# Performance work log

Measured on AMD Instinct MI355X. Metric: run time of the kernel, lower is better.

The kernel has to match this reference:

```python
import jax, jax.numpy as jnp
import numpy as np

GAMMA = 0.99
NUM_CODEWORDS = 512
CODEBOOK_DIM = 64


def setup_inputs() -> dict:
    key = jax.random.key(0)
    kx, kc = jax.random.split(key)
    x = jax.random.normal(kx, (32, 64, 64, 64), dtype=jnp.float32)  # [N,C,H,W]
    codebook = jax.random.normal(kc, (NUM_CODEWORDS, CODEBOOK_DIM), dtype=jnp.float32) / 2
    N_state = jnp.ones((NUM_CODEWORDS,), dtype=jnp.float32)
    m_state = codebook.copy()
    return {"x": x, "codebook": codebook, "N_state": N_state, "m_state": m_state}


def reference(x, codebook, N_state, m_state):
    N, C, H, W = x.shape
    K = codebook.shape[0]
    # flatten to tokens: [N*H*W, C]
    xf = jnp.transpose(x, (0, 2, 3, 1)).reshape(-1, C)
    d2 = (jnp.sum(xf * xf, axis=-1, keepdims=True)
          - 2.0 * (xf @ codebook.T)
          + jnp.sum(codebook * codebook, axis=-1)[None, :])
    index = jnp.argmin(d2, axis=1)  # [T]
    q = codebook[index].reshape(N, H, W, C).transpose(0, 3, 1, 2)  # [N,C,H,W]
    # straight-through estimator
    out = x + jax.lax.stop_gradient(q - x)
    # EMA update (training path, no_grad in original)
    counts = jax.ops.segment_sum(jnp.ones_like(index, dtype=x.dtype), index, num_segments=K)
    sums = jax.ops.segment_sum(xf, index, num_segments=K)  # [K,C]
    occupied = counts > 0
    N_new = jnp.where(occupied, N_state * GAMMA + counts * (1.0 - GAMMA), N_state)
    m_new = jnp.where(occupied[:, None], m_state * GAMMA + sums * (1.0 - GAMMA), m_state)
    codebook_new = m_new / N_new[:, None]
    return out, codebook_new, N_new, m_new
```

## Files before the change

kernel.cpp:

```cpp
#include <hip/hip_runtime.h>

static constexpr int Nn_ = 32, Cc_ = 64, Hh_ = 64, Ww_ = 64;
static constexpr int K_ = 512;
static constexpr int HW_ = Hh_ * Ww_;
static constexpr int CHW_ = Cc_ * HW_;
static constexpr int T_ = Nn_ * Hh_ * Ww_;
static constexpr int OUT_ELEMS = Nn_ * Cc_ * Hh_ * Ww_;
static constexpr int OFF_CB = OUT_ELEMS;
static constexpr int OFF_N  = OUT_ELEMS + 32768;
static constexpr int OFF_M  = OUT_ELEMS + 32768 + 512;

static constexpr int WS_ACC  = 0;
static constexpr int ACC_CNT = 32768;
static constexpr int ACC_F   = K_ * Cc_ + K_;
static constexpr int ZERO4   = ACC_F / 4;

__global__ __launch_bounds__(256) void k_zero(float* __restrict__ ws) {
    int i = blockIdx.x * 256 + threadIdx.x;
    if (i < ZERO4) ((float4*)(ws + WS_ACC))[i] = make_float4(0.f, 0.f, 0.f, 0.f);
}

__global__ __launch_bounds__(256, 2) void k_assign(const float* __restrict__ x,
                                                   const float* __restrict__ cb,
                                                   float* __restrict__ ws,
                                                   float* __restrict__ out) {
    __shared__ alignas(16) float xs[64][132];
    __shared__ alignas(16) float cs[128][68];
    __shared__ float cnorm512[512];
    __shared__ int bi_s[128];

    const int b    = blockIdx.x;
    const int tid  = threadIdx.x;
    const int mg   = tid & 15;
    const int ng   = tid >> 4;
    const int lane = tid & 63;
    const int wv   = tid >> 6;
    const int row0 = 2 * b, row1 = 2 * b + 1;
    const int xb0 = (row0 >> 6) * CHW_ + (row0 & 63) * Ww_;
    const int xb1 = (row1 >> 6) * CHW_ + (row1 & 63) * Ww_;

#pragma unroll
    for (int stp = 0; stp < 8; ++stp) {
        int e = stp * 256 + tid;
        int c = e >> 5, s = e & 31;
        int r = s >> 4, wq = s & 15;
        float4 v = *(const float4*)(x + (r ? xb1 : xb0) + c * HW_ + 4 * wq);
        *(float4*)&xs[c][4 * s] = v;
    }

    for (int r = tid; r < 512; r += 256) {
        const float4* cr = (const float4*)(cb + r * 64);
        float a = 0.f;
#pragma unroll
        for (int i = 0; i < 16; ++i) {
            float4 v = cr[i];
            a = fmaf(v.x, v.x, a); a = fmaf(v.y, v.y, a);
            a = fmaf(v.z, v.z, a); a = fmaf(v.w, v.w, a);
        }
        cnorm512[r] = a;
    }

    float bdA[4], bdB[4];
    int   bkA[4], bkB[4];
#pragma unroll
    for (int i = 0; i < 4; ++i) {
        bdA[i] = __int_as_float(0x7f800000);
        bdB[i] = __int_as_float(0x7f800000);
        bkA[i] = 0; bkB[i] = 0;
    }

#pragma unroll 1
    for (int kt = 0; kt < 4; ++kt) {
#pragma unroll
        for (int stp = 0; stp < 8; ++stp) {
            int e = stp * 256 + tid;
            int rr = e >> 4, cq = e & 15;
            float4 v = *(const float4*)(cb + (kt * 128 + rr) * 64 + 4 * cq);
            *(float4*)&cs[rr][4 * cq] = v;
        }
        __syncthreads();

        float aAA[4][4], aAB[4][4], aBA[4][4], aBB[4][4];
#pragma unroll
        for (int a = 0; a < 4; ++a)
#pragma unroll
            for (int c2 = 0; c2 < 4; ++c2) {
                aAA[a][c2] = 0.f; aAB[a][c2] = 0.f;
                aBA[a][c2] = 0.f; aBB[a][c2] = 0.f;
            }

#pragma unroll 4
        for (int c4 = 0; c4 < 64; c4 += 4) {
            float xA[4][4], xB[4][4], cA[4][4], cB[4][4];
#pragma unroll
            for (int i = 0; i < 4; ++i) {
                *(float4*)xA[i] = *(const float4*)&xs[c4 + i][4 * mg];
                *(float4*)xB[i] = *(const float4*)&xs[c4 + i][64 + 4 * mg];
            }
#pragma unroll
            for (int j = 0; j < 4; ++j) {
                *(float4*)cA[j] = *(const float4*)&cs[4 * ng + j][c4];
                *(float4*)cB[j] = *(const float4*)&cs[64 + 4 * ng + j][c4];
            }
#pragma unroll
            for (int j = 0; j < 4; ++j)
#pragma unroll
                for (int mi = 0; mi < 4; ++mi)
#pragma unroll
                    for (int i = 0; i < 4; ++i) {
                        aAA[mi][j] = fmaf(xA[i][mi], cA[j][i], aAA[mi][j]);
                        aAB[mi][j] = fmaf(xA[i][mi], cB[j][i], aAB[mi][j]);
                        aBA[mi][j] = fmaf(xB[i][mi], cA[j][i], aBA[mi][j]);
                        aBB[mi][j] = fmaf(xB[i][mi], cB[j][i], aBB[mi][j]);
                    }
        }
        __syncthreads();

        const int kb = kt * 128 + 4 * ng;
#pragma unroll
        for (int j = 0; j < 4; ++j) {
            float cn = cnorm512[kb + j];
            int   kk = kb + j;
#pragma unroll
            for (int mi = 0; mi < 4; ++mi) {
                float dA = fmaf(-2.0f, aAA[mi][j], cn);
                if (dA < bdA[mi]) { bdA[mi] = dA; bkA[mi] = kk; }
                float dB = fmaf(-2.0f, aBA[mi][j], cn);
                if (dB < bdB[mi]) { bdB[mi] = dB; bkB[mi] = kk; }
            }
        }
#pragma unroll
        for (int j = 0; j < 4; ++j) {
            float cn = cnorm512[kb + 64 + j];
            int   kk = kb + 64 + j;
#pragma unroll
            for (int mi = 0; mi < 4; ++mi) {
                float dA = fmaf(-2.0f, aAB[mi][j], cn);
                if (dA < bdA[mi]) { bdA[mi] = dA; bkA[mi] = kk; }
                float dB = fmaf(-2.0f, aBB[mi][j], cn);
                if (dB < bdB[mi]) { bdB[mi] = dB; bkB[mi] = kk; }
            }
        }
    }

    unsigned long long* red = (unsigned long long*)&cs[0][0];
#pragma unroll
    for (int mi = 0; mi < 4; ++mi) {
        unsigned uA = __float_as_uint(bdA[mi]);
        uA = (uA & 0x80000000u) ? ~uA : (uA | 0x80000000u);
        red[(4 * mg + mi) * 17 + ng] = ((unsigned long long)uA << 32) | (unsigned)bkA[mi];
        unsigned uB = __float_as_uint(bdB[mi]);
        uB = (uB & 0x80000000u) ? ~uB : (uB | 0x80000000u);
        red[(64 + 4 * mg + mi) * 17 + ng] = ((unsigned long long)uB << 32) | (unsigned)bkB[mi];
    }
    __syncthreads();
    if (tid < 128) {
        unsigned long long bm = red[tid * 17 + 0];
#pragma unroll
        for (int j = 1; j < 16; ++j) {
            unsigned long long v = red[tid * 17 + j];
            if (v < bm) bm = v;
        }
        bi_s[tid] = (int)(bm & 0xffffffffu);
    }
    __syncthreads();

    float* acc = ws + WS_ACC;
#pragma unroll 4
    for (int jj = 0; jj < 32; ++jj) {
        int tt = wv * 32 + jj;
        atomicAdd(acc + bi_s[tt] * 64 + lane, xs[lane][tt]);
    }
    if (tid < 128) atomicAdd(acc + ACC_CNT + bi_s[tid], 1.0f);
    __syncthreads();

    float (*qt)[132] = xs;
#pragma unroll
    for (int jj = 0; jj < 32; ++jj) {
        int tt = wv * 32 + jj;
        qt[lane][tt] = cb[bi_s[tt] * 64 + lane];
    }
    __syncthreads();
#pragma unroll
    for (int r = 0; r < 2; ++r)
#pragma unroll
        for (int j = 0; j < 16; ++j) {
            int c = wv * 16 + j;
            out[(r ? xb1 : xb0) + c * HW_ + lane] = qt[c][64 * r + lane];
        }
}

__global__ __launch_bounds__(256) void k_final(const float* __restrict__ Ns,
                                               const float* __restrict__ ms,
                                               const float* __restrict__ ws,
                                               float* __restrict__ out) {
    int i = blockIdx.x * 256 + threadIdx.x;
    int k = i >> 6, c = i & 63;

    const float* acc = ws + WS_ACC;
    float s   = acc[i];
    float cnt = acc[ACC_CNT + k];

    const float gamma = 0.99f;
    const float omg   = (float)(1.0 - 0.99);

    bool occ = cnt > 0.0f;
    float Nv = Ns[k];
    float Nnew = occ ? (Nv * gamma + cnt * omg) : Nv;

    float mv = ms[i];
    float mnew = occ ? (mv * gamma + s * omg) : mv;

    out[OFF_CB + i] = mnew / Nnew;
    out[OFF_M  + i] = mnew;
    if (c == 0) out[OFF_N + k] = Nnew;
}

extern "C" void kernel_launch(void* const* d_in, const int* in_sizes, int n_in,
                              void* d_out, int out_size, void* d_ws, size_t ws_size,
                              hipStream_t stream) {
    const float* x  = (const float*)d_in[0];
    const float* cb = (const float*)d_in[1];
    const float* Ns = (const float*)d_in[2];
    const float* ms = (const float*)d_in[3];
    float* out = (float*)d_out;
    float* ws  = (float*)d_ws;

    hipLaunchKernelGGL(k_zero,   dim3(33),   dim3(256), 0, stream, ws);
    hipLaunchKernelGGL(k_assign, dim3(1024), dim3(256), 0, stream, x, cb, ws, out);
    hipLaunchKernelGGL(k_final,  dim3(128),  dim3(256), 0, stream, Ns, ms, ws, out);
}
```

Baseline: 217.3 us.

## Compute codeword distances with split-fp16 MFMA and exact fp32 fallback for ambiguous tokens

Replaces the fp32 FMA distance GEMM with 32x32x16 fp16 MFMA using hi/lo split operands (three products) to approximate fp32 dot products. Tokens whose best-vs-second margin is below a threshold are queued and re-evaluated exactly in fp32 by a new fix-up kernel. A prep kernel precomputes split codebook and norms. This aims to cut the compute-bound distance cost at the risk of extra launches and misassignment if the margin is too small.

New measurement: 256.0 us. 17.8% more time.

```diff
diff --git a/kernel.cpp b/kernel.cpp
--- a/kernel.cpp
+++ b/kernel.cpp
@@ -10,171 +10,190 @@
 static constexpr int OFF_N  = OUT_ELEMS + 32768;
 static constexpr int OFF_M  = OUT_ELEMS + 32768 + 512;
 
-static constexpr int WS_ACC  = 0;
-static constexpr int ACC_CNT = 32768;
-static constexpr int ACC_F   = K_ * Cc_ + K_;
-static constexpr int ZERO4   = ACC_F / 4;
+static constexpr int WS_ACC     = 0;
+static constexpr int ACC_CNT    = 32768;
+static constexpr int ACC_F      = K_ * Cc_ + K_;
+static constexpr int WS_FIXCNT  = 33280;
+static constexpr int WS_FIXLIST = 33284;
+static constexpr int WS_CBH     = WS_FIXLIST + T_;
+static constexpr int WS_CBL     = WS_CBH + 16384;
+static constexpr int WS_CN      = WS_CBL + 16384;
+static constexpr int WS_CNA     = WS_CN + 512;
+
+static constexpr float THETA = 0.015f;
+
+typedef _Float16 half8  __attribute__((ext_vector_type(8)));
+typedef float    f32x16 __attribute__((ext_vector_type(16)));
 
 __global__ __launch_bounds__(256) void k_zero(float* __restrict__ ws) {
     int i = blockIdx.x * 256 + threadIdx.x;
-    if (i < ZERO4) ((float4*)(ws + WS_ACC))[i] = make_float4(0.f, 0.f, 0.f, 0.f);
-}
-
-__global__ __launch_bounds__(256, 2) void k_assign(const float* __restrict__ x,
+    if (i < 8321) ((float4*)ws)[i] = make_float4(0.f, 0.f, 0.f, 0.f);
+}
+
+__global__ __launch_bounds__(256) void k_prep(const float* __restrict__ cb,
+                                              float* __restrict__ ws) {
+    int j = blockIdx.x * 256 + threadIdx.x;
+    float v = cb[j];
+    _Float16 h = (_Float16)v;
+    _Float16 lo = (_Float16)(v - (float)h);
+    ((_Float16*)(ws + WS_CBH))[j] = h;
+    ((_Float16*)(ws + WS_CBL))[j] = lo;
+    float sq = v * v;
+#pragma unroll
+    for (int m = 1; m < 64; m <<= 1) sq += __shfl_xor(sq, m);
+    if ((threadIdx.x & 63) == 0) {
+        int k = j >> 6;
+        ws[WS_CN + k] = sq;
+        int t = k >> 5, r5 = k & 31;
+        int hi = (r5 >> 2) & 1;
+        int reg = (r5 & 3) + 4 * (r5 >> 3);
+        ws[WS_CNA + hi * 256 + t * 16 + reg] = sq;
+    }
+}
+
+__global__ __launch_bounds__(256, 4) void k_assign(const float* __restrict__ x,
                                                    const float* __restrict__ cb,
                                                    float* __restrict__ ws,
                                                    float* __restrict__ out) {
-    __shared__ alignas(16) float xs[64][132];
-    __shared__ alignas(16) float cs[128][68];
-    __shared__ float cnorm512[512];
-    __shared__ int bi_s[128];
+    __shared__ alignas(16) unsigned char smem[35840];
+    int* bi_s   = (int*)(smem + 34816);
+    int* cert_s = (int*)(smem + 35328);
 
     const int b    = blockIdx.x;
     const int tid  = threadIdx.x;
-    const int mg   = tid & 15;
-    const int ng   = tid >> 4;
     const int lane = tid & 63;
     const int wv   = tid >> 6;
     const int row0 = 2 * b, row1 = 2 * b + 1;
     const int xb0 = (row0 >> 6) * CHW_ + (row0 & 63) * Ww_;
     const int xb1 = (row1 >> 6) * CHW_ + (row1 & 63) * Ww_;
 
-#pragma unroll
-    for (int stp = 0; stp < 8; ++stp) {
-        int e = stp * 256 + tid;
-        int c = e >> 5, s = e & 31;
-        int r = s >> 4, wq = s & 15;
-        float4 v = *(const float4*)(x + (r ? xb1 : xb0) + c * HW_ + 4 * wq);
-        *(float4*)&xs[c][4 * s] = v;
-    }
-
-    for (int r = tid; r < 512; r += 256) {
-        const float4* cr = (const float4*)(cb + r * 64);
-        float a = 0.f;
-#pragma unroll
-        for (int i = 0; i < 16; ++i) {
-            float4 v = cr[i];
-            a = fmaf(v.x, v.x, a); a = fmaf(v.y, v.y, a);
-            a = fmaf(v.z, v.z, a); a = fmaf(v.w, v.w, a);
-        }
-        cnorm512[r] = a;
-    }
-
-    float bdA[4], bdB[4];
-    int   bkA[4], bkB[4];
-#pragma unroll
-    for (int i = 0; i < 4; ++i) {
-        bdA[i] = __int_as_float(0x7f800000);
-        bdB[i] = __int_as_float(0x7f800000);
-        bkA[i] = 0; bkB[i] = 0;
-    }
+    {
+        const int s  = tid & 31;
+        const int c8 = tid >> 5;
+        const int r  = s >> 4, wq = s & 15;
+        half8 hp[4], lp[4];
+#pragma unroll
+        for (int stp = 0; stp < 8; ++stp) {
+            int ch = c8 * 8 + stp;
+            float4 v = *(const float4*)(x + (r ? xb1 : xb0) + ch * HW_ + 4 * wq);
+            float vv[4] = {v.x, v.y, v.z, v.w};
+#pragma unroll
+            for (int j = 0; j < 4; ++j) {
+                _Float16 h = (_Float16)vv[j];
+                _Float16 lo = (_Float16)(vv[j] - (float)h);
+                hp[j][stp] = h; lp[j][stp] = lo;
+            }
+        }
+        const int blk = c8 ^ (wq & 7);
+#pragma unroll
+        for (int j = 0; j < 4; ++j) {
+            int tt = 64 * r + 4 * wq + j;
+            *(half8*)(smem + tt * 128 + blk * 16) = hp[j];
+            *(half8*)(smem + 16384 + tt * 128 + blk * 16) = lp[j];
+        }
+        ((float*)(smem + 32768))[tid]       = ws[WS_CNA + tid];
+        ((float*)(smem + 32768))[tid + 256] = ws[WS_CNA + tid + 256];
+    }
+    __syncthreads();
+
+    const int tb = 32 * wv + (lane & 31);
+    const int hi = lane >> 5;
+    half8 bh[4], bl[4];
+    {
+        const int tsw = (tb >> 2) & 7;
+#pragma unroll
+        for (int ks = 0; ks < 4; ++ks) {
+            int blk = (2 * ks + hi) ^ tsw;
+            bh[ks] = *(const half8*)(smem + tb * 128 + blk * 16);
+            bl[ks] = *(const half8*)(smem + 16384 + tb * 128 + blk * 16);
+        }
+    }
+
+    const _Float16* __restrict__ cbh = (const _Float16*)(ws + WS_CBH);
+    const _Float16* __restrict__ cbl = (const _Float16*)(ws + WS_CBL);
+    const float* cnA = (const float*)(smem + 32768);
+    float bd1 = __int_as_float(0x7f800000);
+    float bd2 = __int_as_float(0x7f800000);
+    int bk1 = 0;
 
 #pragma unroll 1
-    for (int kt = 0; kt < 4; ++kt) {
-#pragma unroll
-        for (int stp = 0; stp < 8; ++stp) {
-            int e = stp * 256 + tid;
-            int rr = e >> 4, cq = e & 15;
-            float4 v = *(const float4*)(cb + (kt * 128 + rr) * 64 + 4 * cq);
-            *(float4*)&cs[rr][4 * cq] = v;
-        }
-        __syncthreads();
-
-        float aAA[4][4], aAB[4][4], aBA[4][4], aBB[4][4];
-#pragma unroll
-        for (int a = 0; a < 4; ++a)
-#pragma unroll
-            for (int c2 = 0; c2 < 4; ++c2) {
-                aAA[a][c2] = 0.f; aAB[a][c2] = 0.f;
-                aBA[a][c2] = 0.f; aBB[a][c2] = 0.f;
+    for (int t = 0; t < 16; ++t) {
+        const _Float16* ab = cbh + (t * 32 + (lane & 31)) * 64 + 8 * hi;
+        const _Float16* lb = cbl + (t * 32 + (lane & 31)) * 64 + 8 * hi;
+        half8 ah[4], al[4];
+#pragma unroll
+        for (int ks = 0; ks < 4; ++ks) {
+            ah[ks] = *(const half8*)(ab + ks * 16);
+            al[ks] = *(const half8*)(lb + ks * 16);
+        }
+        f32x16 acc = {0.f,0.f,0.f,0.f, 0.f,0.f,0.f,0.f,
+                      0.f,0.f,0.f,0.f, 0.f,0.f,0.f,0.f};
+#pragma unroll
+        for (int ks = 0; ks < 4; ++ks) {
+            acc = __builtin_amdgcn_mfma_f32_32x32x16_f16(ah[ks], bh[ks], acc, 0, 0, 0);
+            acc = __builtin_amdgcn_mfma_f32_32x32x16_f16(ah[ks], bl[ks], acc, 0, 0, 0);
+            acc = __builtin_amdgcn_mfma_f32_32x32x16_f16(al[ks], bh[ks], acc, 0, 0, 0);
+        }
+        float cnv[16];
+        {
+            const float* cnp = cnA + hi * 256 + t * 16;
+            *(float4*)&cnv[0]  = *(const float4*)(cnp);
+            *(float4*)&cnv[4]  = *(const float4*)(cnp + 4);
+            *(float4*)&cnv[8]  = *(const float4*)(cnp + 8);
+            *(float4*)&cnv[12] = *(const float4*)(cnp + 12);
+        }
+        const int tb16 = t << 4;
+#pragma unroll
+        for (int j = 0; j < 16; ++j) {
+            float d = fmaf(-2.0f, acc[j], cnv[j]);
+            int kid = tb16 | j;
+            bool lt = d < bd1;
+            bd2 = lt ? bd1 : fminf(bd2, d);
+            bk1 = lt ? kid : bk1;
+            bd1 = fminf(bd1, d);
+        }
+    }
+
+    {
+        int t0 = bk1 >> 4, j0 = bk1 & 15;
+        int rk = 32 * t0 + (j0 & 3) + 8 * (j0 >> 2) + 4 * hi;
+        unsigned uf = __float_as_uint(bd1);
+        uf = (uf & 0x80000000u) ? ~uf : (uf | 0x80000000u);
+        unsigned long long me = ((unsigned long long)uf << 32) | (unsigned)rk;
+        unsigned long long ot = (unsigned long long)__shfl_xor((long long)me, 32);
+        float od1 = __shfl_xor(bd1, 32);
+        float od2 = __shfl_xor(bd2, 32);
+        unsigned long long m1 = (me < ot) ? me : ot;
+        float d1m = fminf(bd1, od1);
+        float d2m = fminf(fminf(bd2, od2), fmaxf(bd1, od1));
+        if (hi == 0) {
+            int k1 = (int)(m1 & 0xffffffffu);
+            bool cert = (d2m - d1m) > THETA;
+            bi_s[tb] = k1;
+            cert_s[tb] = cert ? 1 : 0;
+            if (!cert) {
+                int pos = atomicAdd((int*)(ws + WS_FIXCNT), 1);
+                ((int*)(ws + WS_FIXLIST))[pos] = 128 * b + tb;
             }
-
-#pragma unroll 4
-        for (int c4 = 0; c4 < 64; c4 += 4) {
-            float xA[4][4], xB[4][4], cA[4][4], cB[4][4];
-#pragma unroll
-            for (int i = 0; i < 4; ++i) {
-                *(float4*)xA[i] = *(const float4*)&xs[c4 + i][4 * mg];
-                *(float4*)xB[i] = *(const float4*)&xs[c4 + i][64 + 4 * mg];
-            }
-#pragma unroll
-            for (int j = 0; j < 4; ++j) {
-                *(float4*)cA[j] = *(const float4*)&cs[4 * ng + j][c4];
-                *(float4*)cB[j] = *(const float4*)&cs[64 + 4 * ng + j][c4];
-            }
-#pragma unroll
-            for (int j = 0; j < 4; ++j)
-#pragma unroll
-                for (int mi = 0; mi < 4; ++mi)
-#pragma unroll
-                    for (int i = 0; i < 4; ++i) {
-                        aAA[mi][j] = fmaf(xA[i][mi], cA[j][i], aAA[mi][j]);
-                        aAB[mi][j] = fmaf(xA[i][mi], cB[j][i], aAB[mi][j]);
-                        aBA[mi][j] = fmaf(xB[i][mi], cA[j][i], aBA[mi][j]);
-                        aBB[mi][j] = fmaf(xB[i][mi], cB[j][i], aBB[mi][j]);
-                    }
-        }
-        __syncthreads();
-
-        const int kb = kt * 128 + 4 * ng;
-#pragma unroll
-        for (int j = 0; j < 4; ++j) {
-            float cn = cnorm512[kb + j];
-            int   kk = kb + j;
-#pragma unroll
-            for (int mi = 0; mi < 4; ++mi) {
-                float dA = fmaf(-2.0f, aAA[mi][j], cn);
-                if (dA < bdA[mi]) { bdA[mi] = dA; bkA[mi] = kk; }
-                float dB = fmaf(-2.0f, aBA[mi][j], cn);
-                if (dB < bdB[mi]) { bdB[mi] = dB; bkB[mi] = kk; }
-            }
-        }
-#pragma unroll
-        for (int j = 0; j < 4; ++j) {
-            float cn = cnorm512[kb + 64 + j];
-            int   kk = kb + 64 + j;
-#pragma unroll
-            for (int mi = 0; mi < 4; ++mi) {
-                float dA = fmaf(-2.0f, aAB[mi][j], cn);
-                if (dA < bdA[mi]) { bdA[mi] = dA; bkA[mi] = kk; }
-                float dB = fmaf(-2.0f, aBB[mi][j], cn);
-                if (dB < bdB[mi]) { bdB[mi] = dB; bkB[mi] = kk; }
-            }
-        }
-    }
-
-    unsigned long long* red = (unsigned long long*)&cs[0][0];
-#pragma unroll
-    for (int mi = 0; mi < 4; ++mi) {
-        unsigned uA = __float_as_uint(bdA[mi]);
-        uA = (uA & 0x80000000u) ? ~uA : (uA | 0x80000000u);
-        red[(4 * mg + mi) * 17 + ng] = ((unsigned long long)uA << 32) | (unsigned)bkA[mi];
-        unsigned uB = __float_as_uint(bdB[mi]);
-        uB = (uB & 0x80000000u) ? ~uB : (uB | 0x80000000u);
-        red[(64 + 4 * mg + mi) * 17 + ng] = ((unsigned long long)uB << 32) | (unsigned)bkB[mi];
+        }
     }
     __syncthreads();
-    if (tid < 128) {
-        unsigned long long bm = red[tid * 17 + 0];
-#pragma unroll
-        for (int j = 1; j < 16; ++j) {
-            unsigned long long v = red[tid * 17 + j];
-            if (v < bm) bm = v;
-        }
-        bi_s[tid] = (int)(bm & 0xffffffffu);
-    }
-    __syncthreads();
-
-    float* acc = ws + WS_ACC;
+
+    float* acc_g = ws + WS_ACC;
 #pragma unroll 4
     for (int jj = 0; jj < 32; ++jj) {
         int tt = wv * 32 + jj;
-        atomicAdd(acc + bi_s[tt] * 64 + lane, xs[lane][tt]);
-    }
-    if (tid < 128) atomicAdd(acc + ACC_CNT + bi_s[tid], 1.0f);
+        if (cert_s[tt]) {
+            int blkS = (lane >> 3) ^ ((tt >> 2) & 7);
+            float xh = (float)*(const _Float16*)(smem + tt * 128 + blkS * 16 + (lane & 7) * 2);
+            float xl = (float)*(const _Float16*)(smem + 16384 + tt * 128 + blkS * 16 + (lane & 7) * 2);
+            atomicAdd(acc_g + bi_s[tt] * 64 + lane, xh + xl);
+        }
+    }
+    if (tid < 128 && cert_s[tid]) atomicAdd(acc_g + ACC_CNT + bi_s[tid], 1.0f);
     __syncthreads();
 
-    float (*qt)[132] = xs;
+    float (*qt)[132] = (float(*)[132])smem;
 #pragma unroll
     for (int jj = 0; jj < 32; ++jj) {
         int tt = wv * 32 + jj;
@@ -188,6 +207,53 @@
             int c = wv * 16 + j;
             out[(r ? xb1 : xb0) + c * HW_ + lane] = qt[c][64 * r + lane];
         }
+}
+
+__global__ __launch_bounds__(256) void k_fix(const float* __restrict__ x,
+                                             const float* __restrict__ cb,
+                                             float* __restrict__ ws,
+                                             float* __restrict__ out) {
+    __shared__ float xw[4][64];
+    const int tid = threadIdx.x, wv = tid >> 6, lane = tid & 63;
+    const int cnt = *(const int*)(ws + WS_FIXCNT);
+    const int* list = (const int*)(ws + WS_FIXLIST);
+
+    for (int it = blockIdx.x * 4 + wv; it < cnt; it += 128 * 4) {
+        int g = list[it];
+        int n = g >> 12, hw = g & 4095;
+        const float* xp = x + n * CHW_ + hw;
+        float xv = xp[lane * HW_];
+        xw[wv][lane] = xv;
+        unsigned long long best = ~0ull;
+#pragma unroll 1
+        for (int jj = 0; jj < 8; ++jj) {
+            int k = lane + 64 * jj;
+            const float4* cr = (const float4*)(cb + k * 64);
+            float dot = 0.f;
+#pragma unroll
+            for (int q = 0; q < 16; ++q) {
+                float4 cv = cr[q];
+                dot = fmaf(cv.x, xw[wv][4 * q + 0], dot);
+                dot = fmaf(cv.y, xw[wv][4 * q + 1], dot);
+                dot = fmaf(cv.z, xw[wv][4 * q + 2], dot);
+                dot = fmaf(cv.w, xw[wv][4 * q + 3], dot);
+            }
+            float d = fmaf(-2.0f, dot, ws[WS_CN + k]);
+            unsigned uf = __float_as_uint(d);
+            uf = (uf & 0x80000000u) ? ~uf : (uf | 0x80000000u);
+            unsigned long long cd = ((unsigned long long)uf << 32) | (unsigned)k;
+            if (cd < best) best = cd;
+        }
+#pragma unroll
+        for (int m = 1; m < 64; m <<= 1) {
+            unsigned long long o = (unsigned long long)__shfl_xor((long long)best, m);
+            if (o < best) best = o;
+        }
+        int k1 = (int)(best & 0xffffffffu);
+        out[n * CHW_ + lane * HW_ + hw] = cb[k1 * 64 + lane];
+        atomicAdd(ws + WS_ACC + k1 * 64 + lane, xw[wv][lane]);
+        if (lane == 0) atomicAdd(ws + WS_ACC + ACC_CNT + k1, 1.0f);
+    }
 }
 
 __global__ __launch_bounds__(256) void k_final(const float* __restrict__ Ns,
@@ -227,6 +293,8 @@
     float* ws  = (float*)d_ws;
 
     hipLaunchKernelGGL(k_zero,   dim3(33),   dim3(256), 0, stream, ws);
+    hipLaunchKernelGGL(k_prep,   dim3(128),  dim3(256), 0, stream, cb, ws);
     hipLaunchKernelGGL(k_assign, dim3(1024), dim3(256), 0, stream, x, cb, ws, out);
+    hipLaunchKernelGGL(k_fix,    dim3(128),  dim3(256), 0, stream, x, cb, ws, out);
     hipLaunchKernelGGL(k_final,  dim3(128),  dim3(256), 0, stream, Ns, ms, ws, out);
 }
```
